# Kernel optimization log

Hardware: AMD Instinct MI355X
Metric: run time of the kernel (lower is better)

The kernel has to match this reference:

```python
import jax, jax.numpy as jnp
import numpy as np

K = 32        # num_classes
NQ = 16384    # num query samples
C = 512       # feature_dim
H_REF = 512   # refinement_net hidden
H_CONF = 256  # confidence_net hidden
NUM_STEPS = 3


def setup_inputs() -> dict:
    key = jax.random.key(0)
    ks = jax.random.split(key, 8)
    s = 0.02
    return {
        "prototypes": jax.random.normal(ks[0], (K, C), jnp.float32),
        "query_features": jax.random.normal(ks[1], (NQ, C), jnp.float32),
        "query_distances": jax.random.uniform(ks[2], (NQ, K), jnp.float32) * 10.0,
        "W1": jax.random.normal(ks[3], (2 * C, H_REF), jnp.float32) * s,
        "b1": jnp.zeros((H_REF,), jnp.float32),
        "W2": jax.random.normal(ks[4], (H_REF, C), jnp.float32) * s,
        "b2": jnp.zeros((C,), jnp.float32),
        "Wc1": jax.random.normal(ks[5], (2 * C, H_CONF), jnp.float32) * s,
        "bc1": jnp.zeros((H_CONF,), jnp.float32),
        "Wc2": jax.random.normal(ks[6], (H_CONF, 1), jnp.float32) * s,
        "bc2": jnp.zeros((1,), jnp.float32),
    }


def reference(prototypes, query_features, query_distances,
              W1, b1, W2, b2, Wc1, bc1, Wc2, bc2):
    # ---- refinement loop (3 steps, sequential in refined prototypes) ----
    refined = prototypes
    for step in range(NUM_STEPS):
        # soft assignments over classes; temperature = step + 1
        soft = jax.nn.softmax(-query_distances / (step + 1.0), axis=-1)  # (NQ, K)
        wsum = jnp.maximum(soft.sum(axis=0), 1e-6)                       # (K,)  clamp(min=1e-6)
        wmean = (soft.T @ query_features) / wsum[:, None]                # (K, C)
        concat = jnp.concatenate([refined, wmean], axis=-1)              # (K, 2C)
        h = jax.nn.relu(concat @ W1 + b1)                                # dropout is identity in eval
        refinement = h @ W2 + b2                                         # (K, C)
        refined = refined + 0.1 * refinement

    # ---- confidence scores: MLP on [proto, query] pairs, mean over queries ----
    # Split first-layer weight into proto half and query half to avoid
    # materializing the (K, NQ, 2C) concat explicitly (same math).
    Wp, Wq = Wc1[:C], Wc1[C:]
    hp = prototypes @ Wp          # (K, H_CONF)
    hq = query_features @ Wq      # (NQ, H_CONF)
    hidden = jax.nn.relu(hp[:, None, :] + hq[None, :, :] + bc1)  # (K, NQ, H_CONF)
    conf = jax.nn.sigmoid(hidden @ Wc2 + bc2)                    # (K, NQ, 1)
    confidence_scores = conf.reshape(K, -1).mean(axis=1)         # (K,)

    return refined, confidence_scores
```

## Files before the change

kernel.cpp:

```cpp
#include <hip/hip_runtime.h>

#define NQg 16384

typedef __attribute__((ext_vector_type(8))) short short8;
typedef __attribute__((ext_vector_type(4))) short short4_t;
typedef __attribute__((ext_vector_type(8))) __bf16 bf16x8;
typedef __attribute__((ext_vector_type(4))) float floatx4;

union S8B8 { short8 s; bf16x8 b; };

__device__ __forceinline__ short f2bf(float f) {
    union { float f; unsigned u; } v; v.f = f;
    unsigned r = v.u + 0x7fffu + ((v.u >> 16) & 1u);
    return (short)(r >> 16);
}
__device__ __forceinline__ float bf2f(short s) {
    union { unsigned u; float f; } v; v.u = ((unsigned)(unsigned short)s) << 16;
    return v.f;
}
__device__ __forceinline__ float bflo(unsigned u) { return __uint_as_float(u << 16); }
__device__ __forceinline__ float bfhi(unsigned u) { return __uint_as_float(u & 0xffff0000u); }

__global__ __launch_bounds__(256) void k_A(const float* __restrict__ qd,
                                           const float* __restrict__ W1, const float* __restrict__ W2,
                                           const float* __restrict__ Wc1, const float* __restrict__ proto,
                                           const float* __restrict__ qf, const float* __restrict__ bc1,
                                           short* __restrict__ softT,
                                           short* __restrict__ W1p, short* __restrict__ W2p,
                                           short* __restrict__ wqp, float* __restrict__ refined,
                                           short* __restrict__ qf2b, float* __restrict__ wmean,
                                           float* __restrict__ hpb,
                                           int* __restrict__ bar, float* __restrict__ dout) {
    int tid = threadIdx.x, bid = blockIdx.x;
    if (bid < 64) {
        int q = bid * 256 + tid;
        float d[32];
        const float4* p = (const float4*)(qd + (size_t)q * 32);
#pragma unroll
        for (int j = 0; j < 8; j++) {
            float4 v = p[j];
            d[4 * j] = v.x; d[4 * j + 1] = v.y; d[4 * j + 2] = v.z; d[4 * j + 3] = v.w;
        }
#pragma unroll
        for (int s = 0; s < 3; s++) {
            float inv = -1.0f / (float)(s + 1);
            float e[32];
            float sum = 0.f;
#pragma unroll
            for (int k = 0; k < 32; k++) { e[k] = __expf(d[k] * inv); sum += e[k]; }
            float r = 1.0f / sum;
#pragma unroll
            for (int k = 0; k < 32; k++)
                softT[(size_t)(s * 32 + k) * NQg + q] = f2bf(e[k] * r);
        }
        return;
    }
    if (bid < 512) {
        int idx = (bid - 64) * 256 + tid;
        if (idx < 65536) {
            int kg = idx >> 9, n = idx & 511;
            short8 o;
#pragma unroll
            for (int j = 0; j < 8; j++) o[j] = f2bf(W1[(size_t)(kg * 8 + j) * 512 + n]);
            *(short8*)&W1p[((size_t)kg * 512 + n) * 8] = o;
        } else if (idx < 98304) {
            int j2 = idx - 65536;
            int kg = j2 >> 9, n = j2 & 511;
            short8 o;
#pragma unroll
            for (int j = 0; j < 8; j++) o[j] = f2bf(W2[(size_t)(kg * 8 + j) * 512 + n]);
            *(short8*)&W2p[((size_t)kg * 512 + n) * 8] = o;
        } else {
            int j3 = idx - 98304;
            int kg = j3 >> 8, n = j3 & 255;
            short8 o;
#pragma unroll
            for (int j = 0; j < 8; j++) o[j] = f2bf(Wc1[(size_t)(512 + kg * 8 + j) * 256 + n]);
            *(short8*)&wqp[((size_t)kg * 256 + n) * 8] = o;
        }
        return;
    }
    if (bid < 576) {
        int idx = (bid - 512) * 256 + tid;
        refined[idx] = proto[idx];
        return;
    }
    if (bid < 768) {
        int idx = (bid - 576) * 256 + tid;
        wmean[idx] = 0.f;
        return;
    }
    if (bid < 2816) {
#pragma unroll
        for (int it = 0; it < 4; it++) {
            int j = (bid - 768) * 1024 + it * 256 + tid;
            float4 v = *(const float4*)&qf[(size_t)j * 4];
            short4_t o;
            o[0] = f2bf(v.x); o[1] = f2bf(v.y); o[2] = f2bf(v.z); o[3] = f2bf(v.w);
            *(short4_t*)&qf2b[(size_t)j * 4] = o;
        }
        return;
    }
    if (bid < 2848) {
        int r = bid - 2816;
        const float* pr = proto + r * 512;
        const float* wc = Wc1 + tid;
        float a0 = 0.f, a1 = 0.f, a2 = 0.f, a3 = 0.f;
#pragma unroll 4
        for (int i = 0; i < 512; i += 4) {
            float4 p4 = *(const float4*)&pr[i];
            float w0 = wc[(size_t)i * 256];
            float w1 = wc[(size_t)(i + 1) * 256];
            float w2 = wc[(size_t)(i + 2) * 256];
            float w3 = wc[(size_t)(i + 3) * 256];
            a0 += p4.x * w0;
            a1 += p4.y * w1;
            a2 += p4.z * w2;
            a3 += p4.w * w3;
        }
        hpb[r * 256 + tid] = bc1[tid] + ((a0 + a1) + (a2 + a3));
        return;
    }
    {
        if (tid < 8) bar[tid] = 0;
        else if (tid >= 32 && tid < 64) dout[16384 + tid - 32] = 0.f;
    }
}

__global__ __launch_bounds__(256) void k_B(const short* __restrict__ qf2b,
                                           const short* __restrict__ softT,
                                           float* __restrict__ wmean,
                                           float* __restrict__ wsuminv,
                                           const short* __restrict__ wqp,
                                           const float* __restrict__ hpb,
                                           const float* __restrict__ Wc2,
                                           const float* __restrict__ bc2p,
                                           float* __restrict__ dout) {
    __shared__ float smem[6688];
    int tid = threadIdx.x;
    int lane = tid & 63, w = tid >> 6;
    int ml = lane & 15, q8 = lane >> 4;
    int bid = blockIdx.x;

    if (bid < 256) {
        short* B_lds = (short*)smem;
        int kc = bid >> 2, ns = bid & 3;
        int c0 = ns * 128;
        int qbase0 = kc * 256;
        int c_l = 2 * lane;
        int q_l = 8 * w;

        floatx4 acc[6][2];
#pragma unroll
        for (int mt = 0; mt < 6; mt++)
#pragma unroll
            for (int nt = 0; nt < 2; nt++) acc[mt][nt] = (floatx4){0.f, 0.f, 0.f, 0.f};

        for (int step = 0; step < 8; step++) {
            int qb = qbase0 + step * 32;
            short8 sA, sB;
#pragma unroll
            for (int i = 0; i < 8; i++) {
                unsigned u = *(const unsigned*)&qf2b[(size_t)(qb + q_l + i) * 512 + c0 + c_l];
                sA[i] = (short)(u & 0xffffu);
                sB[i] = (short)(u >> 16);
            }
            __syncthreads();
            *(short8*)&B_lds[c_l * 40 + q_l] = sA;
            *(short8*)&B_lds[(c_l + 1) * 40 + q_l] = sB;
            S8B8 a[6];
#pragma unroll
            for (int mt = 0; mt < 6; mt++)
                a[mt].s = *(const short8*)&softT[(size_t)(mt * 16 + ml) * NQg + qb + q8 * 8];
            __syncthreads();
#pragma unroll
            for (int nt = 0; nt < 2; nt++) {
                S8B8 b; b.s = *(short8*)&B_lds[(w * 32 + nt * 16 + ml) * 40 + q8 * 8];
#pragma unroll
                for (int mt = 0; mt < 6; mt++)
                    acc[mt][nt] = __builtin_amdgcn_mfma_f32_16x16x32_bf16(a[mt].b, b.b, acc[mt][nt], 0, 0, 0);
            }
        }
        int mrot = kc % 6;
#pragma unroll
        for (int mtt = 0; mtt < 6; mtt++) {
            int mt = mtt + mrot; if (mt >= 6) mt -= 6;
#pragma unroll
            for (int nt = 0; nt < 2; nt++) {
                int c = c0 + w * 32 + nt * 16 + ml;
#pragma unroll
                for (int r = 0; r < 4; r++) {
                    int m = mt * 16 + q8 * 4 + r;
                    atomicAdd(&wmean[(size_t)m * 512 + c], acc[mt][nt][r]);
                }
            }
        }
    } else if (bid < 352) {
        float* red = smem;
        int sk = bid - 256;
        const short* row = softT + (size_t)sk * NQg;
        float s = 0.f;
#pragma unroll
        for (int j = 0; j < 8; j++) {
            short8 v = *(const short8*)&row[j * 2048 + tid * 8];
#pragma unroll
            for (int i = 0; i < 8; i++) s += bf2f(v[i]);
        }
        red[tid] = s;
        __syncthreads();
        for (int off = 128; off > 0; off >>= 1) {
            if (tid < off) red[tid] += red[tid + off];
            __syncthreads();
        }
        if (tid == 0) wsuminv[sk] = 1.0f / fmaxf(red[0], 1e-6f);
    } else {
        short* hq_lds = (short*)smem;
        short* hp_s   = (short*)smem + 4480;
        float* wc2s   = smem + 6400;
        float* confl  = smem + 6656;
        int q0 = (bid - 352) * 16;

        wc2s[tid] = Wc2[tid];
        if (tid < 32) confl[tid] = 0.f;
#pragma unroll
        for (int i = 0; i < 8; i++) {
            int idx = i * 256 + tid;
            int r = idx >> 6, c = (idx & 63) * 4;
            float4 v = *(const float4*)&hpb[r * 256 + c];
            short4_t o;
            o[0] = f2bf(v.x); o[1] = f2bf(v.y); o[2] = f2bf(v.z); o[3] = f2bf(v.w);
            *(short4_t*)&hp_s[r * 260 + c] = o;
        }
        {
            floatx4 acc[4];
#pragma unroll
            for (int nt = 0; nt < 4; nt++) acc[nt] = (floatx4){0.f, 0.f, 0.f, 0.f};
            const short* qa = qf2b + (size_t)(q0 + ml) * 512 + q8 * 8;
#pragma unroll 4
            for (int kc = 0; kc < 512; kc += 32) {
                S8B8 a; a.s = *(const short8*)&qa[kc];
#pragma unroll
                for (int nt = 0; nt < 4; nt++) {
                    int col = w * 64 + nt * 16 + ml;
                    S8B8 b; b.s = *(const short8*)&wqp[((size_t)((kc >> 3) + q8) * 256 + col) * 8];
                    acc[nt] = __builtin_amdgcn_mfma_f32_16x16x32_bf16(a.b, b.b, acc[nt], 0, 0, 0);
                }
            }
#pragma unroll
            for (int nt = 0; nt < 4; nt++)
#pragma unroll
                for (int r = 0; r < 4; r++)
                    hq_lds[(q8 * 4 + r) * 280 + w * 64 + nt * 16 + ml] = f2bf(acc[nt][r]);
        }
        __syncthreads();

        int q = tid & 15, kg = tid >> 4;
        int k0 = kg, k1 = kg + 16;
        float s0 = 0.f, s1 = 0.f;
        for (int h = 0; h < 256; h += 4) {
            uint2 hv = *(uint2*)&hq_lds[q * 280 + h];
            float f0 = bflo(hv.x), f1 = bfhi(hv.x), f2 = bflo(hv.y), f3 = bfhi(hv.y);
            uint2 u0 = *(uint2*)&hp_s[k0 * 260 + h];
            uint2 u1 = *(uint2*)&hp_s[k1 * 260 + h];
            float4 wv = *(float4*)&wc2s[h];
            s0 += fmaxf(bflo(u0.x) + f0, 0.f) * wv.x;
            s0 += fmaxf(bfhi(u0.x) + f1, 0.f) * wv.y;
            s0 += fmaxf(bflo(u0.y) + f2, 0.f) * wv.z;
            s0 += fmaxf(bfhi(u0.y) + f3, 0.f) * wv.w;
            s1 += fmaxf(bflo(u1.x) + f0, 0.f) * wv.x;
            s1 += fmaxf(bfhi(u1.x) + f1, 0.f) * wv.y;
            s1 += fmaxf(bflo(u1.y) + f2, 0.f) * wv.z;
            s1 += fmaxf(bfhi(u1.y) + f3, 0.f) * wv.w;
        }
        float bc2 = bc2p[0];
        float v0 = 1.f / (1.f + __expf(-(s0 + bc2)));
        float v1 = 1.f / (1.f + __expf(-(s1 + bc2)));
        atomicAdd(&confl[k0], v0);
        atomicAdd(&confl[k1], v1);
        __syncthreads();
        if (tid < 32) {
            int cell = (tid + bid) & 31;
            atomicAdd(&dout[16384 + cell], confl[cell] * (1.0f / 16384.0f));
        }
    }
}

__device__ __forceinline__ void gbar(int* bar, int phase, int nblk) {
    __syncthreads();
    if (threadIdx.x == 0) {
        __threadfence();
        __hip_atomic_fetch_add(&bar[phase], 1, __ATOMIC_ACQ_REL, __HIP_MEMORY_SCOPE_AGENT);
        while (__hip_atomic_load(&bar[phase], __ATOMIC_ACQUIRE, __HIP_MEMORY_SCOPE_AGENT) < nblk)
            __builtin_amdgcn_s_sleep(1);
    }
    __syncthreads();
}

__global__ __launch_bounds__(256) void k_D(const float* __restrict__ wmean,
                                           const float* __restrict__ wsuminv,
                                           const short* __restrict__ W1p,
                                           const float* __restrict__ b1,
                                           const short* __restrict__ W2p,
                                           const float* __restrict__ b2,
                                           float* __restrict__ refined,
                                           short* __restrict__ hb,
                                           int* __restrict__ bar,
                                           float* __restrict__ dout) {
    __shared__ float smem[4608];
    int tid = threadIdx.x, lane = tid & 63, w = tid >> 6;
    int ml = lane & 15, q8 = lane >> 4;

    float (*red)[32][36] = (float(*)[32][36])smem;
    int nb = blockIdx.x;
    int phase = 0;
    for (int s = 0; s < 3; s++) {
        {
            const float* srcA = (w < 2) ? refined : (wmean + (size_t)s * 32 * 512 - 512);
            float iv0 = 1.f, iv1 = 1.f;
            if (w >= 2) {
                iv0 = wsuminv[s * 32 + ml];
                iv1 = wsuminv[s * 32 + 16 + ml];
            }
            int kw = w * 256;
            floatx4 acc[2][2];
#pragma unroll
            for (int mt = 0; mt < 2; mt++)
#pragma unroll
                for (int nt = 0; nt < 2; nt++) acc[mt][nt] = (floatx4){0.f, 0.f, 0.f, 0.f};
            for (int st = 0; st < 8; st++) {
                int k0 = kw + st * 32 + q8 * 8;
                S8B8 a[2];
#pragma unroll
                for (int mt = 0; mt < 2; mt++) {
                    float sc = mt ? iv1 : iv0;
                    const float* p = &srcA[(size_t)(mt * 16 + ml) * 512 + k0];
                    float4 f0 = *(const float4*)p;
                    float4 f1 = *(const float4*)(p + 4);
                    short8 t;
                    t[0] = f2bf(f0.x * sc); t[1] = f2bf(f0.y * sc);
                    t[2] = f2bf(f0.z * sc); t[3] = f2bf(f0.w * sc);
                    t[4] = f2bf(f1.x * sc); t[5] = f2bf(f1.y * sc);
                    t[6] = f2bf(f1.z * sc); t[7] = f2bf(f1.w * sc);
                    a[mt].s = t;
                }
#pragma unroll
                for (int nt = 0; nt < 2; nt++) {
                    int n = nb * 32 + nt * 16 + ml;
                    S8B8 b; b.s = *(const short8*)&W1p[((size_t)(k0 >> 3) * 512 + n) * 8];
#pragma unroll
                    for (int mt = 0; mt < 2; mt++)
                        acc[mt][nt] = __builtin_amdgcn_mfma_f32_16x16x32_bf16(a[mt].b, b.b, acc[mt][nt], 0, 0, 0);
                }
            }
            __syncthreads();
#pragma unroll
            for (int mt = 0; mt < 2; mt++)
#pragma unroll
                for (int nt = 0; nt < 2; nt++)
#pragma unroll
                    for (int r = 0; r < 4; r++)
                        red[w][mt * 16 + q8 * 4 + r][nt * 16 + ml] = acc[mt][nt][r];
            __syncthreads();
            int m = tid >> 3, n0 = (tid & 7) * 4;
            short4_t o;
#pragma unroll
            for (int i = 0; i < 4; i++) {
                float v = b1[nb * 32 + n0 + i];
#pragma unroll
                for (int w4 = 0; w4 < 4; w4++) v += red[w4][m][n0 + i];
                o[i] = f2bf(fmaxf(v, 0.f));
            }
            *(short4_t*)&hb[(size_t)m * 512 + nb * 32 + n0] = o;
        }
        gbar(bar, phase++, 16);
        {
            int kw = w * 128;
            floatx4 acc[2][2];
#pragma unroll
            for (int mt = 0; mt < 2; mt++)
#pragma unroll
                for (int nt = 0; nt < 2; nt++) acc[mt][nt] = (floatx4){0.f, 0.f, 0.f, 0.f};
            for (int st = 0; st < 4; st++) {
                int k0 = kw + st * 32 + q8 * 8;
                S8B8 a[2];
#pragma unroll
                for (int mt = 0; mt < 2; mt++)
                    a[mt].s = *(const short8*)&hb[(size_t)(mt * 16 + ml) * 512 + k0];
#pragma unroll
                for (int nt = 0; nt < 2; nt++) {
                    int n = nb * 32 + nt * 16 + ml;
                    S8B8 b; b.s = *(const short8*)&W2p[((size_t)(k0 >> 3) * 512 + n) * 8];
#pragma unroll
                    for (int mt = 0; mt < 2; mt++)
                        acc[mt][nt] = __builtin_amdgcn_mfma_f32_16x16x32_bf16(a[mt].b, b.b, acc[mt][nt], 0, 0, 0);
                }
            }
            __syncthreads();
#pragma unroll
            for (int mt = 0; mt < 2; mt++)
#pragma unroll
                for (int nt = 0; nt < 2; nt++)
#pragma unroll
                    for (int r = 0; r < 4; r++)
                        red[w][mt * 16 + q8 * 4 + r][nt * 16 + ml] = acc[mt][nt][r];
            __syncthreads();
            int m = tid >> 3, n0 = (tid & 7) * 4;
#pragma unroll
            for (int i = 0; i < 4; i++) {
                int c = nb * 32 + n0 + i;
                float v = b2[c];
#pragma unroll
                for (int w4 = 0; w4 < 4; w4++) v += red[w4][m][n0 + i];
                float val = refined[(size_t)m * 512 + c] + 0.1f * v;
                refined[(size_t)m * 512 + c] = val;
                if (s == 2) dout[(size_t)m * 512 + c] = val;
            }
        }
        if (s < 2) gbar(bar, phase++, 16);
    }
}

extern "C" void kernel_launch(void* const* d_in, const int* in_sizes, int n_in,
                              void* d_out, int out_size, void* d_ws, size_t ws_size,
                              hipStream_t stream) {
    const float* proto = (const float*)d_in[0];
    const float* qf    = (const float*)d_in[1];
    const float* qd    = (const float*)d_in[2];
    const float* W1    = (const float*)d_in[3];
    const float* b1    = (const float*)d_in[4];
    const float* W2    = (const float*)d_in[5];
    const float* b2    = (const float*)d_in[6];
    const float* Wc1   = (const float*)d_in[7];
    const float* bc1   = (const float*)d_in[8];
    const float* Wc2   = (const float*)d_in[9];
    const float* bc2   = (const float*)d_in[10];
    float* out = (float*)d_out;

    float* ws = (float*)d_ws;
    short* softT   = (short*)ws;
    short* qf2b    = (short*)(ws + 786432);
    float* wmean   = ws + 4980736;
    float* refined = ws + 5029888;
    short* hb      = (short*)(ws + 5046272);
    short* W1p     = (short*)(ws + 5054464);
    short* W2p     = (short*)(ws + 5316608);
    short* wqp     = (short*)(ws + 5447680);
    float* hpb     = ws + 5513216;
    int*   bar     = (int*)(ws + 5521408);
    float* wsuminv = ws + 5521416;

    k_A<<<2849, 256, 0, stream>>>(qd, W1, W2, Wc1, proto, qf, bc1, softT, W1p, W2p, wqp,
                                  refined, qf2b, wmean, hpb, bar, out);
    k_B<<<1376, 256, 0, stream>>>(qf2b, softT, wmean, wsuminv, wqp, hpb, Wc2, bc2, out);
    k_D<<<16, 256, 0, stream>>>(wmean, wsuminv, W1p, b1, W2p, b2, refined, hb, bar, out);
}
```

Before: 200.7 us.

## Fuse refinement MLP into main kernel and convert query features to bf16 inline

Drops the separate fp32-to-bf16 pass over query_features. The weighted-mean GEMM and the confidence blocks now read fp32 and convert in registers, which saves a write and a re-read of a 16 MB bf16 copy. The former third kernel (the 3-step refinement MLP) becomes the first 16 blocks of k_B. Those blocks spin on an atomic counter until all wmean and wsum producer blocks have signalled, which removes one launch and lets the refinement overlap with the confidence computation. The trade-offs are that the spin-wait blocks hold CUs, correctness relies on the first 16 blocks being co-resident with the producers, and fp32 loads now happen twice (wmean GEMM and confidence).

```diff
diff --git a/kernel.cpp b/kernel.cpp
--- a/kernel.cpp
+++ b/kernel.cpp
@@ -24,12 +24,11 @@
 __global__ __launch_bounds__(256) void k_A(const float* __restrict__ qd,
                                            const float* __restrict__ W1, const float* __restrict__ W2,
                                            const float* __restrict__ Wc1, const float* __restrict__ proto,
-                                           const float* __restrict__ qf, const float* __restrict__ bc1,
+                                           const float* __restrict__ bc1,
                                            short* __restrict__ softT,
                                            short* __restrict__ W1p, short* __restrict__ W2p,
                                            short* __restrict__ wqp, float* __restrict__ refined,
-                                           short* __restrict__ qf2b, float* __restrict__ wmean,
-                                           float* __restrict__ hpb,
+                                           float* __restrict__ wmean, float* __restrict__ hpb,
                                            int* __restrict__ bar, float* __restrict__ dout) {
     int tid = threadIdx.x, bid = blockIdx.x;
     if (bid < 64) {
@@ -90,19 +89,8 @@
         wmean[idx] = 0.f;
         return;
     }
-    if (bid < 2816) {
-#pragma unroll
-        for (int it = 0; it < 4; it++) {
-            int j = (bid - 768) * 1024 + it * 256 + tid;
-            float4 v = *(const float4*)&qf[(size_t)j * 4];
-            short4_t o;
-            o[0] = f2bf(v.x); o[1] = f2bf(v.y); o[2] = f2bf(v.z); o[3] = f2bf(v.w);
-            *(short4_t*)&qf2b[(size_t)j * 4] = o;
-        }
-        return;
-    }
-    if (bid < 2848) {
-        int r = bid - 2816;
+    if (bid < 800) {
+        int r = bid - 768;
         const float* pr = proto + r * 512;
         const float* wc = Wc1 + tid;
         float a0 = 0.f, a1 = 0.f, a2 = 0.f, a3 = 0.f;
@@ -127,7 +115,18 @@
     }
 }
 
-__global__ __launch_bounds__(256) void k_B(const short* __restrict__ qf2b,
+__device__ __forceinline__ void gbar(int* bar, int phase, int nblk) {
+    __syncthreads();
+    if (threadIdx.x == 0) {
+        __threadfence();
+        __hip_atomic_fetch_add(&bar[phase], 1, __ATOMIC_ACQ_REL, __HIP_MEMORY_SCOPE_AGENT);
+        while (__hip_atomic_load(&bar[phase], __ATOMIC_ACQUIRE, __HIP_MEMORY_SCOPE_AGENT) < nblk)
+            __builtin_amdgcn_s_sleep(1);
+    }
+    __syncthreads();
+}
+
+__global__ __launch_bounds__(256) void k_B(const float* __restrict__ qf,
                                            const short* __restrict__ softT,
                                            float* __restrict__ wmean,
                                            float* __restrict__ wsuminv,
@@ -135,6 +134,13 @@
                                            const float* __restrict__ hpb,
                                            const float* __restrict__ Wc2,
                                            const float* __restrict__ bc2p,
+                                           const short* __restrict__ W1p,
+                                           const float* __restrict__ b1,
+                                           const short* __restrict__ W2p,
+                                           const float* __restrict__ b2,
+                                           float* __restrict__ refined,
+                                           short* __restrict__ hb,
+                                           int* __restrict__ bar,
                                            float* __restrict__ dout) {
     __shared__ float smem[6688];
     int tid = threadIdx.x;
@@ -142,9 +148,126 @@
     int ml = lane & 15, q8 = lane >> 4;
     int bid = blockIdx.x;
 
-    if (bid < 256) {
+    if (bid < 16) {
+        if (tid == 0) {
+            while (__hip_atomic_load(&bar[7], __ATOMIC_ACQUIRE, __HIP_MEMORY_SCOPE_AGENT) < 352)
+                __builtin_amdgcn_s_sleep(1);
+        }
+        __syncthreads();
+        float (*red)[32][36] = (float(*)[32][36])smem;
+        int nb = bid;
+        int phase = 0;
+        for (int s = 0; s < 3; s++) {
+            {
+                const float* srcA = (w < 2) ? refined : (wmean + (size_t)s * 32 * 512 - 512);
+                float iv0 = 1.f, iv1 = 1.f;
+                if (w >= 2) {
+                    iv0 = wsuminv[s * 32 + ml];
+                    iv1 = wsuminv[s * 32 + 16 + ml];
+                }
+                int kw = w * 256;
+                floatx4 acc[2][2];
+#pragma unroll
+                for (int mt = 0; mt < 2; mt++)
+#pragma unroll
+                    for (int nt = 0; nt < 2; nt++) acc[mt][nt] = (floatx4){0.f, 0.f, 0.f, 0.f};
+                for (int st = 0; st < 8; st++) {
+                    int k0 = kw + st * 32 + q8 * 8;
+                    S8B8 a[2];
+#pragma unroll
+                    for (int mt = 0; mt < 2; mt++) {
+                        float sc = mt ? iv1 : iv0;
+                        const float* p = &srcA[(size_t)(mt * 16 + ml) * 512 + k0];
+                        float4 f0 = *(const float4*)p;
+                        float4 f1 = *(const float4*)(p + 4);
+                        short8 t;
+                        t[0] = f2bf(f0.x * sc); t[1] = f2bf(f0.y * sc);
+                        t[2] = f2bf(f0.z * sc); t[3] = f2bf(f0.w * sc);
+                        t[4] = f2bf(f1.x * sc); t[5] = f2bf(f1.y * sc);
+                        t[6] = f2bf(f1.z * sc); t[7] = f2bf(f1.w * sc);
+                        a[mt].s = t;
+                    }
+#pragma unroll
+                    for (int nt = 0; nt < 2; nt++) {
+                        int n = nb * 32 + nt * 16 + ml;
+                        S8B8 b; b.s = *(const short8*)&W1p[((size_t)(k0 >> 3) * 512 + n) * 8];
+#pragma unroll
+                        for (int mt = 0; mt < 2; mt++)
+                            acc[mt][nt] = __builtin_amdgcn_mfma_f32_16x16x32_bf16(a[mt].b, b.b, acc[mt][nt], 0, 0, 0);
+                    }
+                }
+                __syncthreads();
+#pragma unroll
+                for (int mt = 0; mt < 2; mt++)
+#pragma unroll
+                    for (int nt = 0; nt < 2; nt++)
+#pragma unroll
+                        for (int r = 0; r < 4; r++)
+                            red[w][mt * 16 + q8 * 4 + r][nt * 16 + ml] = acc[mt][nt][r];
+                __syncthreads();
+                int m = tid >> 3, n0 = (tid & 7) * 4;
+                short4_t o;
+#pragma unroll
+                for (int i = 0; i < 4; i++) {
+                    float v = b1[nb * 32 + n0 + i];
+#pragma unroll
+                    for (int w4 = 0; w4 < 4; w4++) v += red[w4][m][n0 + i];
+                    o[i] = f2bf(fmaxf(v, 0.f));
+                }
+                *(short4_t*)&hb[(size_t)m * 512 + nb * 32 + n0] = o;
+            }
+            gbar(bar, phase++, 16);
+            {
+                int kw = w * 128;
+                floatx4 acc[2][2];
+#pragma unroll
+                for (int mt = 0; mt < 2; mt++)
+#pragma unroll
+                    for (int nt = 0; nt < 2; nt++) acc[mt][nt] = (floatx4){0.f, 0.f, 0.f, 0.f};
+                for (int st = 0; st < 4; st++) {
+                    int k0 = kw + st * 32 + q8 * 8;
+                    S8B8 a[2];
+#pragma unroll
+                    for (int mt = 0; mt < 2; mt++)
+                        a[mt].s = *(const short8*)&hb[(size_t)(mt * 16 + ml) * 512 + k0];
+#pragma unroll
+                    for (int nt = 0; nt < 2; nt++) {
+                        int n = nb * 32 + nt * 16 + ml;
+                        S8B8 b; b.s = *(const short8*)&W2p[((size_t)(k0 >> 3) * 512 + n) * 8];
+#pragma unroll
+                        for (int mt = 0; mt < 2; mt++)
+                            acc[mt][nt] = __builtin_amdgcn_mfma_f32_16x16x32_bf16(a[mt].b, b.b, acc[mt][nt], 0, 0, 0);
+                    }
+                }
+                __syncthreads();
+#pragma unroll
+                for (int mt = 0; mt < 2; mt++)
+#pragma unroll
+                    for (int nt = 0; nt < 2; nt++)
+#pragma unroll
+                        for (int r = 0; r < 4; r++)
+                            red[w][mt * 16 + q8 * 4 + r][nt * 16 + ml] = acc[mt][nt][r];
+                __syncthreads();
+                int m = tid >> 3, n0 = (tid & 7) * 4;
+#pragma unroll
+                for (int i = 0; i < 4; i++) {
+                    int c = nb * 32 + n0 + i;
+                    float v = b2[c];
+#pragma unroll
+                    for (int w4 = 0; w4 < 4; w4++) v += red[w4][m][n0 + i];
+                    float val = refined[(size_t)m * 512 + c] + 0.1f * v;
+                    refined[(size_t)m * 512 + c] = val;
+                    if (s == 2) dout[(size_t)m * 512 + c] = val;
+                }
+            }
+            if (s < 2) gbar(bar, phase++, 16);
+        }
+        return;
+    }
+
+    if (bid < 272) {
         short* B_lds = (short*)smem;
-        int kc = bid >> 2, ns = bid & 3;
+        int kc = (bid - 16) >> 2, ns = (bid - 16) & 3;
         int c0 = ns * 128;
         int qbase0 = kc * 256;
         int c_l = 2 * lane;
@@ -161,9 +284,9 @@
             short8 sA, sB;
 #pragma unroll
             for (int i = 0; i < 8; i++) {
-                unsigned u = *(const unsigned*)&qf2b[(size_t)(qb + q_l + i) * 512 + c0 + c_l];
-                sA[i] = (short)(u & 0xffffu);
-                sB[i] = (short)(u >> 16);
+                float2 u = *(const float2*)&qf[(size_t)(qb + q_l + i) * 512 + c0 + c_l];
+                sA[i] = f2bf(u.x);
+                sB[i] = f2bf(u.y);
             }
             __syncthreads();
             *(short8*)&B_lds[c_l * 40 + q_l] = sA;
@@ -181,10 +304,8 @@
                     acc[mt][nt] = __builtin_amdgcn_mfma_f32_16x16x32_bf16(a[mt].b, b.b, acc[mt][nt], 0, 0, 0);
             }
         }
-        int mrot = kc % 6;
-#pragma unroll
-        for (int mtt = 0; mtt < 6; mtt++) {
-            int mt = mtt + mrot; if (mt >= 6) mt -= 6;
+#pragma unroll
+        for (int mt = 0; mt < 6; mt++) {
 #pragma unroll
             for (int nt = 0; nt < 2; nt++) {
                 int c = c0 + w * 32 + nt * 16 + ml;
@@ -195,9 +316,17 @@
                 }
             }
         }
-    } else if (bid < 352) {
+        __syncthreads();
+        if (tid == 0) {
+            __threadfence();
+            __hip_atomic_fetch_add(&bar[7], 1, __ATOMIC_ACQ_REL, __HIP_MEMORY_SCOPE_AGENT);
+        }
+        return;
+    }
+
+    if (bid < 368) {
         float* red = smem;
-        int sk = bid - 256;
+        int sk = bid - 272;
         const short* row = softT + (size_t)sk * NQg;
         float s = 0.f;
 #pragma unroll
@@ -212,13 +341,20 @@
             if (tid < off) red[tid] += red[tid + off];
             __syncthreads();
         }
-        if (tid == 0) wsuminv[sk] = 1.0f / fmaxf(red[0], 1e-6f);
-    } else {
+        if (tid == 0) {
+            wsuminv[sk] = 1.0f / fmaxf(red[0], 1e-6f);
+            __threadfence();
+            __hip_atomic_fetch_add(&bar[7], 1, __ATOMIC_ACQ_REL, __HIP_MEMORY_SCOPE_AGENT);
+        }
+        return;
+    }
+
+    {
         short* hq_lds = (short*)smem;
         short* hp_s   = (short*)smem + 4480;
         float* wc2s   = smem + 6400;
         float* confl  = smem + 6656;
-        int q0 = (bid - 352) * 16;
+        int q0 = (bid - 368) * 16;
 
         wc2s[tid] = Wc2[tid];
         if (tid < 32) confl[tid] = 0.f;
@@ -235,10 +371,15 @@
             floatx4 acc[4];
 #pragma unroll
             for (int nt = 0; nt < 4; nt++) acc[nt] = (floatx4){0.f, 0.f, 0.f, 0.f};
-            const short* qa = qf2b + (size_t)(q0 + ml) * 512 + q8 * 8;
+            const float* qfa = qf + (size_t)(q0 + ml) * 512 + q8 * 8;
 #pragma unroll 4
             for (int kc = 0; kc < 512; kc += 32) {
-                S8B8 a; a.s = *(const short8*)&qa[kc];
+                float4 fa = *(const float4*)&qfa[kc];
+                float4 fb = *(const float4*)&qfa[kc + 4];
+                short8 t;
+                t[0] = f2bf(fa.x); t[1] = f2bf(fa.y); t[2] = f2bf(fa.z); t[3] = f2bf(fa.w);
+                t[4] = f2bf(fb.x); t[5] = f2bf(fb.y); t[6] = f2bf(fb.z); t[7] = f2bf(fb.w);
+                S8B8 a; a.s = t;
 #pragma unroll
                 for (int nt = 0; nt < 4; nt++) {
                     int col = w * 64 + nt * 16 + ml;
@@ -285,141 +426,6 @@
     }
 }
 
-__device__ __forceinline__ void gbar(int* bar, int phase, int nblk) {
-    __syncthreads();
-    if (threadIdx.x == 0) {
-        __threadfence();
-        __hip_atomic_fetch_add(&bar[phase], 1, __ATOMIC_ACQ_REL, __HIP_MEMORY_SCOPE_AGENT);
-        while (__hip_atomic_load(&bar[phase], __ATOMIC_ACQUIRE, __HIP_MEMORY_SCOPE_AGENT) < nblk)
-            __builtin_amdgcn_s_sleep(1);
-    }
-    __syncthreads();
-}
-
-__global__ __launch_bounds__(256) void k_D(const float* __restrict__ wmean,
-                                           const float* __restrict__ wsuminv,
-                                           const short* __restrict__ W1p,
-                                           const float* __restrict__ b1,
-                                           const short* __restrict__ W2p,
-                                           const float* __restrict__ b2,
-                                           float* __restrict__ refined,
-                                           short* __restrict__ hb,
-                                           int* __restrict__ bar,
-                                           float* __restrict__ dout) {
-    __shared__ float smem[4608];
-    int tid = threadIdx.x, lane = tid & 63, w = tid >> 6;
-    int ml = lane & 15, q8 = lane >> 4;
-
-    float (*red)[32][36] = (float(*)[32][36])smem;
-    int nb = blockIdx.x;
-    int phase = 0;
-    for (int s = 0; s < 3; s++) {
-        {
-            const float* srcA = (w < 2) ? refined : (wmean + (size_t)s * 32 * 512 - 512);
-            float iv0 = 1.f, iv1 = 1.f;
-            if (w >= 2) {
-                iv0 = wsuminv[s * 32 + ml];
-                iv1 = wsuminv[s * 32 + 16 + ml];
-            }
-            int kw = w * 256;
-            floatx4 acc[2][2];
-#pragma unroll
-            for (int mt = 0; mt < 2; mt++)
-#pragma unroll
-                for (int nt = 0; nt < 2; nt++) acc[mt][nt] = (floatx4){0.f, 0.f, 0.f, 0.f};
-            for (int st = 0; st < 8; st++) {
-                int k0 = kw + st * 32 + q8 * 8;
-                S8B8 a[2];
-#pragma unroll
-                for (int mt = 0; mt < 2; mt++) {
-                    float sc = mt ? iv1 : iv0;
-                    const float* p = &srcA[(size_t)(mt * 16 + ml) * 512 + k0];
-                    float4 f0 = *(const float4*)p;
-                    float4 f1 = *(const float4*)(p + 4);
-                    short8 t;
-                    t[0] = f2bf(f0.x * sc); t[1] = f2bf(f0.y * sc);
-                    t[2] = f2bf(f0.z * sc); t[3] = f2bf(f0.w * sc);
-                    t[4] = f2bf(f1.x * sc); t[5] = f2bf(f1.y * sc);
-                    t[6] = f2bf(f1.z * sc); t[7] = f2bf(f1.w * sc);
-                    a[mt].s = t;
-                }
-#pragma unroll
-                for (int nt = 0; nt < 2; nt++) {
-                    int n = nb * 32 + nt * 16 + ml;
-                    S8B8 b; b.s = *(const short8*)&W1p[((size_t)(k0 >> 3) * 512 + n) * 8];
-#pragma unroll
-                    for (int mt = 0; mt < 2; mt++)
-                        acc[mt][nt] = __builtin_amdgcn_mfma_f32_16x16x32_bf16(a[mt].b, b.b, acc[mt][nt], 0, 0, 0);
-                }
-            }
-            __syncthreads();
-#pragma unroll
-            for (int mt = 0; mt < 2; mt++)
-#pragma unroll
-                for (int nt = 0; nt < 2; nt++)
-#pragma unroll
-                    for (int r = 0; r < 4; r++)
-                        red[w][mt * 16 + q8 * 4 + r][nt * 16 + ml] = acc[mt][nt][r];
-            __syncthreads();
-            int m = tid >> 3, n0 = (tid & 7) * 4;
-            short4_t o;
-#pragma unroll
-            for (int i = 0; i < 4; i++) {
-                float v = b1[nb * 32 + n0 + i];
-#pragma unroll
-                for (int w4 = 0; w4 < 4; w4++) v += red[w4][m][n0 + i];
-                o[i] = f2bf(fmaxf(v, 0.f));
-            }
-            *(short4_t*)&hb[(size_t)m * 512 + nb * 32 + n0] = o;
-        }
-        gbar(bar, phase++, 16);
-        {
-            int kw = w * 128;
-            floatx4 acc[2][2];
-#pragma unroll
-            for (int mt = 0; mt < 2; mt++)
-#pragma unroll
-                for (int nt = 0; nt < 2; nt++) acc[mt][nt] = (floatx4){0.f, 0.f, 0.f, 0.f};
-            for (int st = 0; st < 4; st++) {
-                int k0 = kw + st * 32 + q8 * 8;
-                S8B8 a[2];
-#pragma unroll
-                for (int mt = 0; mt < 2; mt++)
-                    a[mt].s = *(const short8*)&hb[(size_t)(mt * 16 + ml) * 512 + k0];
-#pragma unroll
-                for (int nt = 0; nt < 2; nt++) {
-                    int n = nb * 32 + nt * 16 + ml;
-                    S8B8 b; b.s = *(const short8*)&W2p[((size_t)(k0 >> 3) * 512 + n) * 8];
-#pragma unroll
-                    for (int mt = 0; mt < 2; mt++)
-                        acc[mt][nt] = __builtin_amdgcn_mfma_f32_16x16x32_bf16(a[mt].b, b.b, acc[mt][nt], 0, 0, 0);
-                }
-            }
-            __syncthreads();
-#pragma unroll
-            for (int mt = 0; mt < 2; mt++)
-#pragma unroll
-                for (int nt = 0; nt < 2; nt++)
-#pragma unroll
-                    for (int r = 0; r < 4; r++)
-                        red[w][mt * 16 + q8 * 4 + r][nt * 16 + ml] = acc[mt][nt][r];
-            __syncthreads();
-            int m = tid >> 3, n0 = (tid & 7) * 4;
-#pragma unroll
-            for (int i = 0; i < 4; i++) {
-                int c = nb * 32 + n0 + i;
-                float v = b2[c];
-#pragma unroll
-                for (int w4 = 0; w4 < 4; w4++) v += red[w4][m][n0 + i];
-                float val = refined[(size_t)m * 512 + c] + 0.1f * v;
-                refined[(size_t)m * 512 + c] = val;
-                if (s == 2) dout[(size_t)m * 512 + c] = val;
-            }
-        }
-        if (s < 2) gbar(bar, phase++, 16);
-    }
-}
-
 extern "C" void kernel_launch(void* const* d_in, const int* in_sizes, int n_in,
                               void* d_out, int out_size, void* d_ws, size_t ws_size,
                               hipStream_t stream) {
@@ -438,19 +444,18 @@
 
     float* ws = (float*)d_ws;
     short* softT   = (short*)ws;
-    short* qf2b    = (short*)(ws + 786432);
-    float* wmean   = ws + 4980736;
-    float* refined = ws + 5029888;
-    short* hb      = (short*)(ws + 5046272);
-    short* W1p     = (short*)(ws + 5054464);
-    short* W2p     = (short*)(ws + 5316608);
-    short* wqp     = (short*)(ws + 5447680);
-    float* hpb     = ws + 5513216;
-    int*   bar     = (int*)(ws + 5521408);
-    float* wsuminv = ws + 5521416;
-
-    k_A<<<2849, 256, 0, stream>>>(qd, W1, W2, Wc1, proto, qf, bc1, softT, W1p, W2p, wqp,
-                                  refined, qf2b, wmean, hpb, bar, out);
-    k_B<<<1376, 256, 0, stream>>>(qf2b, softT, wmean, wsuminv, wqp, hpb, Wc2, bc2, out);
-    k_D<<<16, 256, 0, stream>>>(wmean, wsuminv, W1p, b1, W2p, b2, refined, hb, bar, out);
-}
+    float* wmean   = ws + 786432;
+    float* refined = ws + 835584;
+    short* hb      = (short*)(ws + 851968);
+    short* W1p     = (short*)(ws + 860160);
+    short* W2p     = (short*)(ws + 1122304);
+    short* wqp     = (short*)(ws + 1253376);
+    float* hpb     = ws + 1318912;
+    int*   bar     = (int*)(ws + 1327104);
+    float* wsuminv = ws + 1327112;
+
+    k_A<<<801, 256, 0, stream>>>(qd, W1, W2, Wc1, proto, bc1, softT, W1p, W2p, wqp,
+                                 refined, wmean, hpb, bar, out);
+    k_B<<<1392, 256, 0, stream>>>(qf, softT, wmean, wsuminv, wqp, hpb, Wc2, bc2,
+                                  W1p, b1, W2p, b2, refined, hb, bar, out);
+}
```

New measurement: 181.0 us. -9.8%, faster.

## Fuse refinement MLP into k_B via atomic counter to overlap with confidence work

Applied to the files above, without the earlier changes.

Merges the 16-block refinement kernel into k_B as its first 16 blocks. These spin on a global counter that the weighted-mean and wsum blocks increment when they finish, so the serial refinement chain overlaps with the confidence-score blocks and one kernel launch is dropped. The change also removes the rotation of atomic write order in the wmean accumulation. It relies on the first 16 blocks being co-resident with the producer blocks, which risks deadlock if they are scheduled first and occupy slots the producers need. It also adds contention from the spinning blocks.

```diff
diff --git a/kernel.cpp b/kernel.cpp
--- a/kernel.cpp
+++ b/kernel.cpp
@@ -127,24 +127,159 @@
     }
 }
 
-__global__ __launch_bounds__(256) void k_B(const short* __restrict__ qf2b,
-                                           const short* __restrict__ softT,
-                                           float* __restrict__ wmean,
-                                           float* __restrict__ wsuminv,
-                                           const short* __restrict__ wqp,
-                                           const float* __restrict__ hpb,
-                                           const float* __restrict__ Wc2,
-                                           const float* __restrict__ bc2p,
-                                           float* __restrict__ dout) {
+__device__ __forceinline__ void gbar(int* bar, int phase, int nblk) {
+    __syncthreads();
+    if (threadIdx.x == 0) {
+        __threadfence();
+        __hip_atomic_fetch_add(&bar[phase], 1, __ATOMIC_ACQ_REL, __HIP_MEMORY_SCOPE_AGENT);
+        while (__hip_atomic_load(&bar[phase], __ATOMIC_ACQUIRE, __HIP_MEMORY_SCOPE_AGENT) < nblk)
+            __builtin_amdgcn_s_sleep(1);
+    }
+    __syncthreads();
+}
+
+__global__ __launch_bounds__(256, 4) void k_B(const short* __restrict__ qf2b,
+                                              const short* __restrict__ softT,
+                                              float* __restrict__ wmean,
+                                              float* __restrict__ wsuminv,
+                                              const short* __restrict__ wqp,
+                                              const float* __restrict__ hpb,
+                                              const float* __restrict__ Wc2,
+                                              const float* __restrict__ bc2p,
+                                              const short* __restrict__ W1p,
+                                              const float* __restrict__ b1,
+                                              const short* __restrict__ W2p,
+                                              const float* __restrict__ b2,
+                                              float* __restrict__ refined,
+                                              short* __restrict__ hb,
+                                              int* __restrict__ bar,
+                                              float* __restrict__ dout) {
     __shared__ float smem[6688];
     int tid = threadIdx.x;
     int lane = tid & 63, w = tid >> 6;
     int ml = lane & 15, q8 = lane >> 4;
     int bid = blockIdx.x;
 
-    if (bid < 256) {
+    if (bid < 16) {
+        if (tid == 0) {
+            while (__hip_atomic_load(&bar[7], __ATOMIC_ACQUIRE, __HIP_MEMORY_SCOPE_AGENT) < 352)
+                __builtin_amdgcn_s_sleep(1);
+        }
+        __syncthreads();
+        float (*red)[32][36] = (float(*)[32][36])smem;
+        int nb = bid;
+        int phase = 0;
+        for (int s = 0; s < 3; s++) {
+            {
+                const float* srcA = (w < 2) ? refined : (wmean + (size_t)s * 32 * 512 - 512);
+                float iv0 = 1.f, iv1 = 1.f;
+                if (w >= 2) {
+                    iv0 = wsuminv[s * 32 + ml];
+                    iv1 = wsuminv[s * 32 + 16 + ml];
+                }
+                int kw = w * 256;
+                floatx4 acc[2][2];
+#pragma unroll
+                for (int mt = 0; mt < 2; mt++)
+#pragma unroll
+                    for (int nt = 0; nt < 2; nt++) acc[mt][nt] = (floatx4){0.f, 0.f, 0.f, 0.f};
+                for (int st = 0; st < 8; st++) {
+                    int k0 = kw + st * 32 + q8 * 8;
+                    S8B8 a[2];
+#pragma unroll
+                    for (int mt = 0; mt < 2; mt++) {
+                        float sc = mt ? iv1 : iv0;
+                        const float* p = &srcA[(size_t)(mt * 16 + ml) * 512 + k0];
+                        float4 f0 = *(const float4*)p;
+                        float4 f1 = *(const float4*)(p + 4);
+                        short8 t;
+                        t[0] = f2bf(f0.x * sc); t[1] = f2bf(f0.y * sc);
+                        t[2] = f2bf(f0.z * sc); t[3] = f2bf(f0.w * sc);
+                        t[4] = f2bf(f1.x * sc); t[5] = f2bf(f1.y * sc);
+                        t[6] = f2bf(f1.z * sc); t[7] = f2bf(f1.w * sc);
+                        a[mt].s = t;
+                    }
+#pragma unroll
+                    for (int nt = 0; nt < 2; nt++) {
+                        int n = nb * 32 + nt * 16 + ml;
+                        S8B8 b; b.s = *(const short8*)&W1p[((size_t)(k0 >> 3) * 512 + n) * 8];
+#pragma unroll
+                        for (int mt = 0; mt < 2; mt++)
+                            acc[mt][nt] = __builtin_amdgcn_mfma_f32_16x16x32_bf16(a[mt].b, b.b, acc[mt][nt], 0, 0, 0);
+                    }
+                }
+                __syncthreads();
+#pragma unroll
+                for (int mt = 0; mt < 2; mt++)
+#pragma unroll
+                    for (int nt = 0; nt < 2; nt++)
+#pragma unroll
+                        for (int r = 0; r < 4; r++)
+                            red[w][mt * 16 + q8 * 4 + r][nt * 16 + ml] = acc[mt][nt][r];
+                __syncthreads();
+                int m = tid >> 3, n0 = (tid & 7) * 4;
+                short4_t o;
+#pragma unroll
+                for (int i = 0; i < 4; i++) {
+                    float v = b1[nb * 32 + n0 + i];
+#pragma unroll
+                    for (int w4 = 0; w4 < 4; w4++) v += red[w4][m][n0 + i];
+                    o[i] = f2bf(fmaxf(v, 0.f));
+                }
+                *(short4_t*)&hb[(size_t)m * 512 + nb * 32 + n0] = o;
+            }
+            gbar(bar, phase++, 16);
+            {
+                int kw = w * 128;
+                floatx4 acc[2][2];
+#pragma unroll
+                for (int mt = 0; mt < 2; mt++)
+#pragma unroll
+                    for (int nt = 0; nt < 2; nt++) acc[mt][nt] = (floatx4){0.f, 0.f, 0.f, 0.f};
+                for (int st = 0; st < 4; st++) {
+                    int k0 = kw + st * 32 + q8 * 8;
+                    S8B8 a[2];
+#pragma unroll
+                    for (int mt = 0; mt < 2; mt++)
+                        a[mt].s = *(const short8*)&hb[(size_t)(mt * 16 + ml) * 512 + k0];
+#pragma unroll
+                    for (int nt = 0; nt < 2; nt++) {
+                        int n = nb * 32 + nt * 16 + ml;
+                        S8B8 b; b.s = *(const short8*)&W2p[((size_t)(k0 >> 3) * 512 + n) * 8];
+#pragma unroll
+                        for (int mt = 0; mt < 2; mt++)
+                            acc[mt][nt] = __builtin_amdgcn_mfma_f32_16x16x32_bf16(a[mt].b, b.b, acc[mt][nt], 0, 0, 0);
+                    }
+                }
+                __syncthreads();
+#pragma unroll
+                for (int mt = 0; mt < 2; mt++)
+#pragma unroll
+                    for (int nt = 0; nt < 2; nt++)
+#pragma unroll
+                        for (int r = 0; r < 4; r++)
+                            red[w][mt * 16 + q8 * 4 + r][nt * 16 + ml] = acc[mt][nt][r];
+                __syncthreads();
+                int m = tid >> 3, n0 = (tid & 7) * 4;
+#pragma unroll
+                for (int i = 0; i < 4; i++) {
+                    int c = nb * 32 + n0 + i;
+                    float v = b2[c];
+#pragma unroll
+                    for (int w4 = 0; w4 < 4; w4++) v += red[w4][m][n0 + i];
+                    float val = refined[(size_t)m * 512 + c] + 0.1f * v;
+                    refined[(size_t)m * 512 + c] = val;
+                    if (s == 2) dout[(size_t)m * 512 + c] = val;
+                }
+            }
+            if (s < 2) gbar(bar, phase++, 16);
+        }
+        return;
+    }
+
+    if (bid < 272) {
         short* B_lds = (short*)smem;
-        int kc = bid >> 2, ns = bid & 3;
+        int kc = (bid - 16) >> 2, ns = (bid - 16) & 3;
         int c0 = ns * 128;
         int qbase0 = kc * 256;
         int c_l = 2 * lane;
@@ -181,10 +316,8 @@
                     acc[mt][nt] = __builtin_amdgcn_mfma_f32_16x16x32_bf16(a[mt].b, b.b, acc[mt][nt], 0, 0, 0);
             }
         }
-        int mrot = kc % 6;
-#pragma unroll
-        for (int mtt = 0; mtt < 6; mtt++) {
-            int mt = mtt + mrot; if (mt >= 6) mt -= 6;
+#pragma unroll
+        for (int mt = 0; mt < 6; mt++) {
 #pragma unroll
             for (int nt = 0; nt < 2; nt++) {
                 int c = c0 + w * 32 + nt * 16 + ml;
@@ -195,9 +328,17 @@
                 }
             }
         }
-    } else if (bid < 352) {
+        __syncthreads();
+        if (tid == 0) {
+            __threadfence();
+            __hip_atomic_fetch_add(&bar[7], 1, __ATOMIC_ACQ_REL, __HIP_MEMORY_SCOPE_AGENT);
+        }
+        return;
+    }
+
+    if (bid < 368) {
         float* red = smem;
-        int sk = bid - 256;
+        int sk = bid - 272;
         const short* row = softT + (size_t)sk * NQg;
         float s = 0.f;
 #pragma unroll
@@ -212,13 +353,20 @@
             if (tid < off) red[tid] += red[tid + off];
             __syncthreads();
         }
-        if (tid == 0) wsuminv[sk] = 1.0f / fmaxf(red[0], 1e-6f);
-    } else {
+        if (tid == 0) {
+            wsuminv[sk] = 1.0f / fmaxf(red[0], 1e-6f);
+            __threadfence();
+            __hip_atomic_fetch_add(&bar[7], 1, __ATOMIC_ACQ_REL, __HIP_MEMORY_SCOPE_AGENT);
+        }
+        return;
+    }
+
+    {
         short* hq_lds = (short*)smem;
         short* hp_s   = (short*)smem + 4480;
         float* wc2s   = smem + 6400;
         float* confl  = smem + 6656;
-        int q0 = (bid - 352) * 16;
+        int q0 = (bid - 368) * 16;
 
         wc2s[tid] = Wc2[tid];
         if (tid < 32) confl[tid] = 0.f;
@@ -285,141 +433,6 @@
     }
 }
 
-__device__ __forceinline__ void gbar(int* bar, int phase, int nblk) {
-    __syncthreads();
-    if (threadIdx.x == 0) {
-        __threadfence();
-        __hip_atomic_fetch_add(&bar[phase], 1, __ATOMIC_ACQ_REL, __HIP_MEMORY_SCOPE_AGENT);
-        while (__hip_atomic_load(&bar[phase], __ATOMIC_ACQUIRE, __HIP_MEMORY_SCOPE_AGENT) < nblk)
-            __builtin_amdgcn_s_sleep(1);
-    }
-    __syncthreads();
-}
-
-__global__ __launch_bounds__(256) void k_D(const float* __restrict__ wmean,
-                                           const float* __restrict__ wsuminv,
-                                           const short* __restrict__ W1p,
-                                           const float* __restrict__ b1,
-                                           const short* __restrict__ W2p,
-                                           const float* __restrict__ b2,
-                                           float* __restrict__ refined,
-                                           short* __restrict__ hb,
-                                           int* __restrict__ bar,
-                                           float* __restrict__ dout) {
-    __shared__ float smem[4608];
-    int tid = threadIdx.x, lane = tid & 63, w = tid >> 6;
-    int ml = lane & 15, q8 = lane >> 4;
-
-    float (*red)[32][36] = (float(*)[32][36])smem;
-    int nb = blockIdx.x;
-    int phase = 0;
-    for (int s = 0; s < 3; s++) {
-        {
-            const float* srcA = (w < 2) ? refined : (wmean + (size_t)s * 32 * 512 - 512);
-            float iv0 = 1.f, iv1 = 1.f;
-            if (w >= 2) {
-                iv0 = wsuminv[s * 32 + ml];
-                iv1 = wsuminv[s * 32 + 16 + ml];
-            }
-            int kw = w * 256;
-            floatx4 acc[2][2];
-#pragma unroll
-            for (int mt = 0; mt < 2; mt++)
-#pragma unroll
-                for (int nt = 0; nt < 2; nt++) acc[mt][nt] = (floatx4){0.f, 0.f, 0.f, 0.f};
-            for (int st = 0; st < 8; st++) {
-                int k0 = kw + st * 32 + q8 * 8;
-                S8B8 a[2];
-#pragma unroll
-                for (int mt = 0; mt < 2; mt++) {
-                    float sc = mt ? iv1 : iv0;
-                    const float* p = &srcA[(size_t)(mt * 16 + ml) * 512 + k0];
-                    float4 f0 = *(const float4*)p;
-                    float4 f1 = *(const float4*)(p + 4);
-                    short8 t;
-                    t[0] = f2bf(f0.x * sc); t[1] = f2bf(f0.y * sc);
-                    t[2] = f2bf(f0.z * sc); t[3] = f2bf(f0.w * sc);
-                    t[4] = f2bf(f1.x * sc); t[5] = f2bf(f1.y * sc);
-                    t[6] = f2bf(f1.z * sc); t[7] = f2bf(f1.w * sc);
-                    a[mt].s = t;
-                }
-#pragma unroll
-                for (int nt = 0; nt < 2; nt++) {
-                    int n = nb * 32 + nt * 16 + ml;
-                    S8B8 b; b.s = *(const short8*)&W1p[((size_t)(k0 >> 3) * 512 + n) * 8];
-#pragma unroll
-                    for (int mt = 0; mt < 2; mt++)
-                        acc[mt][nt] = __builtin_amdgcn_mfma_f32_16x16x32_bf16(a[mt].b, b.b, acc[mt][nt], 0, 0, 0);
-                }
-            }
-            __syncthreads();
-#pragma unroll
-            for (int mt = 0; mt < 2; mt++)
-#pragma unroll
-                for (int nt = 0; nt < 2; nt++)
-#pragma unroll
-                    for (int r = 0; r < 4; r++)
-                        red[w][mt * 16 + q8 * 4 + r][nt * 16 + ml] = acc[mt][nt][r];
-            __syncthreads();
-            int m = tid >> 3, n0 = (tid & 7) * 4;
-            short4_t o;
-#pragma unroll
-            for (int i = 0; i < 4; i++) {
-                float v = b1[nb * 32 + n0 + i];
-#pragma unroll
-                for (int w4 = 0; w4 < 4; w4++) v += red[w4][m][n0 + i];
-                o[i] = f2bf(fmaxf(v, 0.f));
-            }
-            *(short4_t*)&hb[(size_t)m * 512 + nb * 32 + n0] = o;
-        }
-        gbar(bar, phase++, 16);
-        {
-            int kw = w * 128;
-            floatx4 acc[2][2];
-#pragma unroll
-            for (int mt = 0; mt < 2; mt++)
-#pragma unroll
-                for (int nt = 0; nt < 2; nt++) acc[mt][nt] = (floatx4){0.f, 0.f, 0.f, 0.f};
-            for (int st = 0; st < 4; st++) {
-                int k0 = kw + st * 32 + q8 * 8;
-                S8B8 a[2];
-#pragma unroll
-                for (int mt = 0; mt < 2; mt++)
-                    a[mt].s = *(const short8*)&hb[(size_t)(mt * 16 + ml) * 512 + k0];
-#pragma unroll
-                for (int nt = 0; nt < 2; nt++) {
-                    int n = nb * 32 + nt * 16 + ml;
-                    S8B8 b; b.s = *(const short8*)&W2p[((size_t)(k0 >> 3) * 512 + n) * 8];
-#pragma unroll
-                    for (int mt = 0; mt < 2; mt++)
-                        acc[mt][nt] = __builtin_amdgcn_mfma_f32_16x16x32_bf16(a[mt].b, b.b, acc[mt][nt], 0, 0, 0);
-                }
-            }
-            __syncthreads();
-#pragma unroll
-            for (int mt = 0; mt < 2; mt++)
-#pragma unroll
-                for (int nt = 0; nt < 2; nt++)
-#pragma unroll
-                    for (int r = 0; r < 4; r++)
-                        red[w][mt * 16 + q8 * 4 + r][nt * 16 + ml] = acc[mt][nt][r];
-            __syncthreads();
-            int m = tid >> 3, n0 = (tid & 7) * 4;
-#pragma unroll
-            for (int i = 0; i < 4; i++) {
-                int c = nb * 32 + n0 + i;
-                float v = b2[c];
-#pragma unroll
-                for (int w4 = 0; w4 < 4; w4++) v += red[w4][m][n0 + i];
-                float val = refined[(size_t)m * 512 + c] + 0.1f * v;
-                refined[(size_t)m * 512 + c] = val;
-                if (s == 2) dout[(size_t)m * 512 + c] = val;
-            }
-        }
-        if (s < 2) gbar(bar, phase++, 16);
-    }
-}
-
 extern "C" void kernel_launch(void* const* d_in, const int* in_sizes, int n_in,
                               void* d_out, int out_size, void* d_ws, size_t ws_size,
                               hipStream_t stream) {
@@ -451,6 +464,6 @@
 
     k_A<<<2849, 256, 0, stream>>>(qd, W1, W2, Wc1, proto, qf, bc1, softT, W1p, W2p, wqp,
                                   refined, qf2b, wmean, hpb, bar, out);
-    k_B<<<1376, 256, 0, stream>>>(qf2b, softT, wmean, wsuminv, wqp, hpb, Wc2, bc2, out);
-    k_D<<<16, 256, 0, stream>>>(wmean, wsuminv, W1p, b1, W2p, b2, refined, hb, bar, out);
-}
+    k_B<<<1392, 256, 0, stream>>>(qf2b, softT, wmean, wsuminv, wqp, hpb, Wc2, bc2,
+                                  W1p, b1, W2p, b2, refined, hb, bar, out);
+}
```

New measurement: 198.5 us. No clear change (-1.1%).
